# Optimization experiments

Measured on AMD Instinct MI355X. Metric: run time of the kernel, lower is better.

Reference implementation:

```python
import jax, jax.numpy as jnp
import numpy as np
import math

N_FEATURES = 64
GAMMA_ORDER = 0.5
ALPHA, BETA, ETA = 0.3, 0.4, 0.3
MAX_K = 50


def _make_coeffs():
    # gamma_values[0] = Gamma(g+1); gamma_values[m] (m>=1) = Gamma(m)*Gamma(g-m+2)
    g0 = math.gamma(GAMMA_ORDER + 1.0)
    coeffs = np.zeros(MAX_K + 1, dtype=np.float32)
    coeffs[0] = 1.0
    for k in range(1, MAX_K + 1):
        gv_k = math.gamma(k) * math.gamma(GAMMA_ORDER - k + 2.0)
        coeffs[k] = ((-1.0) ** k) * g0 / gv_k
    return jnp.asarray(coeffs)


def setup_inputs() -> dict:
    key = jax.random.key(0)
    k1, k2, k3, k4 = jax.random.split(key, 4)
    B, T, F = 4, 8192, N_FEATURES
    x = jax.random.normal(k1, (B, T, F), dtype=jnp.float32)
    weight_matrix = jax.random.normal(k2, (F, F), dtype=jnp.float32)
    bound = 1.0 / math.sqrt(F)
    proj_w = jax.random.uniform(k3, (F, F), dtype=jnp.float32, minval=-bound, maxval=bound)
    proj_b = jax.random.uniform(k4, (F,), dtype=jnp.float32, minval=-bound, maxval=bound)
    kappa = jnp.float32(0.1)
    coeffs = _make_coeffs()
    return {"x": x, "weight_matrix": weight_matrix, "proj_w": proj_w,
            "proj_b": proj_b, "kappa": kappa, "coeffs": coeffs}


def _fractional_derivative(x, coeffs):
    # causal conv: result[:, t, :] = sum_{k=0}^{min(t, max_k)} coeffs[k] * x[:, t-k, :]
    K = coeffs.shape[0]
    F = x.shape[-1]
    # depthwise 1D cross-correlation; kernel reversed so it implements x[t-k]
    kern = jnp.tile(coeffs[::-1][:, None, None], (1, 1, F))  # [K, 1, F]
    return jax.lax.conv_general_dilated(
        x, kern, window_strides=(1,), padding=[(K - 1, 0)],
        dimension_numbers=("NWC", "WIO", "NWC"), feature_group_count=F)


def reference(x, weight_matrix, proj_w, proj_b, kappa, coeffs):
    B, T, F = x.shape
    # 1) memory term: fractional derivative (causal conv)
    memory_term = _fractional_derivative(x, coeffs)

    # 2) coupling term: sum_j w[i,j] * tanh(x_i - x_j) * sigmoid(|x_i| + |x_j|)
    #    diagonal contributes tanh(0)=0, matching the i != j skip in the original.
    w = jax.nn.softmax(weight_matrix, axis=1)                 # [F, F]
    xi = x[..., :, None]                                      # [B, T, F, 1]
    xj = x[..., None, :]                                      # [B, T, 1, F]
    c = jnp.tanh(xi - xj) * jax.nn.sigmoid(jnp.abs(xi) + jnp.abs(xj))  # [B,T,F,F]
    coupling_term = jnp.einsum("btij,ij->bti", c, w)

    # 3) global term: proj(x[:, t]) * sum_{s=0}^{t} exp(-kappa * s)
    proj = x @ proj_w.T + proj_b                               # [B, T, F]
    kernel_cumsum = jnp.cumsum(jnp.exp(-kappa * jnp.arange(T, dtype=x.dtype)))
    global_term = proj * kernel_cumsum[None, :, None]

    output = ALPHA * memory_term + BETA * coupling_term + ETA * global_term
    return (output, memory_term)
```

## Files before the change

kernel.cpp:

```cpp
#include <hip/hip_runtime.h>
#include <hip/hip_fp16.h>
#include <math.h>

#define TT 8192
#define FF 64
#define TILE 64
#define HALO 50

typedef float f32x2 __attribute__((ext_vector_type(2)));
typedef float f32x4 __attribute__((ext_vector_type(4)));

__device__ __forceinline__ float rcpf(float x) { return __builtin_amdgcn_rcpf(x); }

__global__ void prep_kernel(const float* __restrict__ W, const float* __restrict__ PW,
                            float* __restrict__ wsmT, float* __restrict__ pwT) {
    const int lane = threadIdx.x;
    const int wv   = threadIdx.y;
    for (int it = 0; it < 16; ++it) {
        const int r = wv * 16 + it;
        float v = W[r * 64 + lane];
        float m = v;
        #pragma unroll
        for (int off = 32; off >= 1; off >>= 1)
            m = fmaxf(m, __shfl_xor(m, off, 64));
        float e = __expf(v - m);
        float s = e;
        #pragma unroll
        for (int off = 32; off >= 1; off >>= 1)
            s += __shfl_xor(s, off, 64);
        wsmT[lane * 64 + r] = e * rcpf(s);
        pwT[lane * 64 + r]  = PW[r * 64 + lane];
    }
}

__global__ __launch_bounds__(1024, 8)
void mcao_main(const float* __restrict__ x,
               const float* __restrict__ wsmT,
               const float* __restrict__ pwT,
               const float* __restrict__ pb,
               const float* __restrict__ kap,
               const float* __restrict__ coeffs,
               float* __restrict__ out,
               float* __restrict__ memout) {
    __shared__ __align__(16) char smem[66048];
    float* xs  = (float*)smem;
    f32x2* tux = (f32x2*)smem;
    float* P2  = (float*)smem;
    float* wS  = (float*)(smem + 33280);
    float* pwS = (float*)(smem + 49664);

    const int tid  = threadIdx.x;
    const int lane = tid & 63;
    const int wv   = tid >> 6;

    const int sw = ((int)blockIdx.x & 7) * 64 + ((int)blockIdx.x >> 3);
    const int b  = sw >> 7;
    const int t0 = (sw & 127) * TILE;
    const float* xb = x + (size_t)b * TT * FF;

    #pragma unroll
    for (int k = 0; k < 2; ++k) {
        const int i4 = tid + 1024 * k;
        if (i4 < 114 * 16) {
            const int s = i4 >> 4, f4 = i4 & 15, t = t0 - HALO + s;
            f32x4 v = {0.f, 0.f, 0.f, 0.f};
            if (t >= 0) v = *(const f32x4*)(xb + (size_t)t * 64 + f4 * 4);
            *(f32x4*)(&xs[s * 64 + f4 * 4]) = v;
        }
    }
    ((f32x4*)wS)[tid]  = ((const f32x4*)wsmT)[tid];
    ((f32x4*)pwS)[tid] = ((const f32x4*)pwT)[tid];
    __syncthreads();

    float macc[4] = {0.f, 0.f, 0.f, 0.f};
    #pragma unroll
    for (int s = 0; s < 54; ++s) {
        const float xv = xs[(4 * wv + s) * 64 + lane];
        #pragma unroll
        for (int r = 0; r < 4; ++r) {
            const int k = r + 50 - s;
            if (0 <= k && k <= 50) macc[r] = fmaf(coeffs[k], xv, macc[r]);
        }
    }
    #pragma unroll
    for (int r = 0; r < 4; ++r)
        memout[(size_t)(b * TT + t0 + 4 * wv + r) * 64 + lane] = macc[r];

    const int erow = tid >> 4, f0 = (tid & 15) * 4;
    const f32x4 xv4 = *(const f32x4*)(&xs[(HALO + erow) * 64 + f0]);
    float tq[4]; unsigned pk[4];
    #pragma unroll
    for (int q = 0; q < 4; ++q) {
        const float xi = xv4[q];
        tq[q] = fmaf(-2.f, rcpf(__expf(2.f * xi) + 1.f), 1.f);
        const float uu = __expf(-fabsf(xi));
        pk[q] = (unsigned)__half_as_ushort(__float2half_rn(xi)) << 16 |
                (unsigned)__half_as_ushort(__float2half_rn(uu));
    }
    __syncthreads();
    #pragma unroll
    for (int q = 0; q < 4; ++q) {
        f32x2 e; e.x = tq[q]; e.y = __uint_as_float(pk[q]);
        tux[(f0 + q) * 65 + erow] = e;
    }
    __syncthreads();

    const int r  = lane;
    const int ib = __builtin_amdgcn_readfirstlane(wv) * 4;

    f32x2 tiP[2], uiP[2];
    #pragma unroll
    for (int q = 0; q < 4; ++q) {
        const f32x2 e = tux[(ib + q) * 65 + r];
        const unsigned u = __float_as_uint(e.y);
        tiP[q >> 1][q & 1] = e.x;
        uiP[q >> 1][q & 1] = __half2float(__ushort_as_half((unsigned short)(u & 0xFFFF)));
    }

    f32x2 cac[2] = {{0.f, 0.f}, {0.f, 0.f}};
    f32x2 pac[2] = {{0.f, 0.f}, {0.f, 0.f}};
    const f32x2 one2 = {1.f, 1.f};
    #pragma unroll 8
    for (int j = 0; j < 64; ++j) {
        const f32x2 e = tux[j * 65 + r];
        const unsigned u = __float_as_uint(e.y);
        const float tj = e.x;
        const float uj = __half2float(__ushort_as_half((unsigned short)(u & 0xFFFF)));
        const float xj = __half2float(__ushort_as_half((unsigned short)(u >> 16)));
        const f32x4 w4 = *(const f32x4*)(wS  + j * 64 + ib);
        const f32x4 p4 = *(const f32x4*)(pwS + j * 64 + ib);
        const f32x2 tjj = {tj, tj}, ujj = {uj, uj}, xjj = {xj, xj};
        #pragma unroll
        for (int g = 0; g < 2; ++g) {
            const f32x2 d1  = __builtin_elementwise_fma(-tiP[g], tjj, one2);
            const f32x2 d2  = __builtin_elementwise_fma( uiP[g], ujj, one2);
            const f32x2 den = d1 * d2;
            f32x2 rr; rr.x = rcpf(den.x); rr.y = rcpf(den.y);
            const f32x2 s = (tiP[g] - tjj) * rr;
            f32x2 wg; wg.x = w4[2 * g]; wg.y = w4[2 * g + 1];
            f32x2 pg; pg.x = p4[2 * g]; pg.y = p4[2 * g + 1];
            cac[g] = __builtin_elementwise_fma(s,   wg, cac[g]);
            pac[g] = __builtin_elementwise_fma(xjj, pg, pac[g]);
        }
    }

    const float kappa  = kap[0];
    const float inv1mr = rcpf(1.f - __expf(-kappa));
    const float ksum   = (1.f - __expf(-kappa * (float)(t0 + r + 1))) * inv1mr;
    const f32x4 pbv    = *(const f32x4*)(pb + ib);
    __syncthreads();
    #pragma unroll
    for (int q = 0; q < 4; ++q) {
        const float cv = (q & 1) ? cac[q >> 1].y : cac[q >> 1].x;
        const float pv = (q & 1) ? pac[q >> 1].y : pac[q >> 1].x;
        P2[(ib + q) * 65 + r] = fmaf(0.4f, cv, 0.3f * (pv + pbv[q]) * ksum);
    }
    __syncthreads();

    #pragma unroll
    for (int rr2 = 0; rr2 < 4; ++rr2) {
        const int row = 4 * wv + rr2;
        out[(size_t)(b * TT + t0 + row) * 64 + lane] =
            fmaf(0.3f, macc[rr2], P2[lane * 65 + row]);
    }
}

extern "C" void kernel_launch(void* const* d_in, const int* in_sizes, int n_in,
                              void* d_out, int out_size, void* d_ws, size_t ws_size,
                              hipStream_t stream) {
    const float* x   = (const float*)d_in[0];
    const float* W   = (const float*)d_in[1];
    const float* PW  = (const float*)d_in[2];
    const float* pb  = (const float*)d_in[3];
    const float* kap = (const float*)d_in[4];
    const float* cf  = (const float*)d_in[5];

    float* out    = (float*)d_out;
    float* memout = out + (size_t)4 * TT * FF;

    float* wsmT = (float*)d_ws;
    float* pwT  = wsmT + 64 * 64;

    hipLaunchKernelGGL(prep_kernel, dim3(1), dim3(64, 4), 0, stream, W, PW, wsmT, pwT);
    hipLaunchKernelGGL(mcao_main, dim3(4 * (TT / TILE)), dim3(1024), 0, stream,
                       x, wsmT, pwT, pb, kap, cf, out, memout);
}
```

Baseline: 48.42 us.

## Compute projection with fp16 MFMA, halve tile size, keep coupling inputs in fp32

Moves the x @ proj_w^T projection out of the scalar inner loop onto 16x16x32 fp16 MFMA instructions, using a B-fragment layout pre-packed by the prep kernel. The tile shrinks from 64 to 32 timesteps with 512-thread blocks, so the grid doubles and LDS use drops, and the P2 buffer switches to an XOR-swizzled layout. tanh and exp(-|x|) are now stored as fp32 rather than packed halves, so the coupling inputs keep full precision. The cost is fp16 rounding of x and proj_w in the projection, plus more halo reloading per output row because the tile is smaller.

```diff
diff --git a/kernel.cpp b/kernel.cpp
--- a/kernel.cpp
+++ b/kernel.cpp
@@ -4,18 +4,21 @@
 
 #define TT 8192
 #define FF 64
-#define TILE 64
+#define TILE 32
 #define HALO 50
 
 typedef float f32x2 __attribute__((ext_vector_type(2)));
 typedef float f32x4 __attribute__((ext_vector_type(4)));
+typedef _Float16 f16x8 __attribute__((ext_vector_type(8)));
+typedef unsigned int u32x4 __attribute__((ext_vector_type(4)));
 
 __device__ __forceinline__ float rcpf(float x) { return __builtin_amdgcn_rcpf(x); }
 
 __global__ void prep_kernel(const float* __restrict__ W, const float* __restrict__ PW,
-                            float* __restrict__ wsmT, float* __restrict__ pwT) {
+                            float* __restrict__ wsmT, u32x4* __restrict__ pwB) {
     const int lane = threadIdx.x;
     const int wv   = threadIdx.y;
+    const int tid  = wv * 64 + lane;
     for (int it = 0; it < 16; ++it) {
         const int r = wv * 16 + it;
         float v = W[r * 64 + lane];
@@ -29,47 +32,55 @@
         for (int off = 32; off >= 1; off >>= 1)
             s += __shfl_xor(s, off, 64);
         wsmT[lane * 64 + r] = e * rcpf(s);
-        pwT[lane * 64 + r]  = PW[r * 64 + lane];
+    }
+    for (int s = tid; s < 512; s += 256) {
+        const int n2 = s >> 6;
+        const int ln = s & 63;
+        const int i  = (n2 >> 1) * 16 + (ln & 15);
+        const int k0 = (n2 & 1) * 32 + (ln >> 4) * 8;
+        u32x4 frag;
+        #pragma unroll
+        for (int w = 0; w < 4; ++w) {
+            const unsigned lo = __half_as_ushort(__float2half_rn(PW[i * 64 + k0 + 2 * w]));
+            const unsigned hi = __half_as_ushort(__float2half_rn(PW[i * 64 + k0 + 2 * w + 1]));
+            frag[w] = lo | (hi << 16);
+        }
+        pwB[s] = frag;
     }
 }
 
-__global__ __launch_bounds__(1024, 8)
+__global__ __launch_bounds__(512, 4)
 void mcao_main(const float* __restrict__ x,
                const float* __restrict__ wsmT,
-               const float* __restrict__ pwT,
+               const u32x4* __restrict__ pwB,
                const float* __restrict__ pb,
                const float* __restrict__ kap,
                const float* __restrict__ coeffs,
                float* __restrict__ out,
                float* __restrict__ memout) {
-    __shared__ __align__(16) char smem[66048];
+    __shared__ __align__(16) char smem[40960];
     float* xs  = (float*)smem;
     f32x2* tux = (f32x2*)smem;
-    float* P2  = (float*)smem;
-    float* wS  = (float*)(smem + 33280);
-    float* pwS = (float*)(smem + 49664);
+    float* P2  = (float*)(smem + 16384);
+    float* wS  = (float*)(smem + 24576);
 
     const int tid  = threadIdx.x;
     const int lane = tid & 63;
     const int wv   = tid >> 6;
 
-    const int sw = ((int)blockIdx.x & 7) * 64 + ((int)blockIdx.x >> 3);
-    const int b  = sw >> 7;
-    const int t0 = (sw & 127) * TILE;
+    const int sw = ((int)blockIdx.x & 7) * 128 + ((int)blockIdx.x >> 3);
+    const int b  = sw >> 8;
+    const int t0 = (sw & 255) * TILE;
     const float* xb = x + (size_t)b * TT * FF;
 
-    #pragma unroll
-    for (int k = 0; k < 2; ++k) {
-        const int i4 = tid + 1024 * k;
-        if (i4 < 114 * 16) {
-            const int s = i4 >> 4, f4 = i4 & 15, t = t0 - HALO + s;
-            f32x4 v = {0.f, 0.f, 0.f, 0.f};
-            if (t >= 0) v = *(const f32x4*)(xb + (size_t)t * 64 + f4 * 4);
-            *(f32x4*)(&xs[s * 64 + f4 * 4]) = v;
-        }
-    }
-    ((f32x4*)wS)[tid]  = ((const f32x4*)wsmT)[tid];
-    ((f32x4*)pwS)[tid] = ((const f32x4*)pwT)[tid];
+    for (int i4 = tid; i4 < 82 * 16; i4 += 512) {
+        const int s = i4 >> 4, f4 = i4 & 15, t = t0 - HALO + s;
+        f32x4 v = {0.f, 0.f, 0.f, 0.f};
+        if (t >= 0) v = *(const f32x4*)(xb + (size_t)t * 64 + f4 * 4);
+        *(f32x4*)(&xs[i4 * 4]) = v;
+    }
+    ((f32x4*)wS)[tid]       = ((const f32x4*)wsmT)[tid];
+    ((f32x4*)wS)[tid + 512] = ((const f32x4*)wsmT)[tid + 512];
     __syncthreads();
 
     float macc[4] = {0.f, 0.f, 0.f, 0.f};
@@ -88,72 +99,97 @@
 
     const int erow = tid >> 4, f0 = (tid & 15) * 4;
     const f32x4 xv4 = *(const f32x4*)(&xs[(HALO + erow) * 64 + f0]);
-    float tq[4]; unsigned pk[4];
+    f32x2 tu[4];
     #pragma unroll
     for (int q = 0; q < 4; ++q) {
         const float xi = xv4[q];
-        tq[q] = fmaf(-2.f, rcpf(__expf(2.f * xi) + 1.f), 1.f);
-        const float uu = __expf(-fabsf(xi));
-        pk[q] = (unsigned)__half_as_ushort(__float2half_rn(xi)) << 16 |
-                (unsigned)__half_as_ushort(__float2half_rn(uu));
-    }
-    __syncthreads();
+        tu[q].x = fmaf(-2.f, rcpf(__expf(2.f * xi) + 1.f), 1.f);
+        tu[q].y = __expf(-fabsf(xi));
+    }
+
+    const int mt = wv >> 2, nt = wv & 3;
+    const int arow = HALO + mt * 16 + (lane & 15);
+    const int kcol = (lane >> 4) * 8;
+    f32x4 cfr = {0.f, 0.f, 0.f, 0.f};
+    #pragma unroll
+    for (int kt = 0; kt < 2; ++kt) {
+        const f32x4 alo = *(const f32x4*)(&xs[arow * 64 + kt * 32 + kcol]);
+        const f32x4 ahi = *(const f32x4*)(&xs[arow * 64 + kt * 32 + kcol + 4]);
+        f16x8 afr;
+        #pragma unroll
+        for (int q = 0; q < 4; ++q) {
+            afr[q]     = (_Float16)alo[q];
+            afr[q + 4] = (_Float16)ahi[q];
+        }
+        const u32x4 bw = pwB[(nt * 2 + kt) * 64 + lane];
+        const f16x8 bfr = __builtin_bit_cast(f16x8, bw);
+        cfr = __builtin_amdgcn_mfma_f32_16x16x32_f16(afr, bfr, cfr, 0, 0, 0);
+    }
+    __syncthreads();
+
+    #pragma unroll
+    for (int q = 0; q < 4; ++q)
+        tux[(f0 + q) * 32 + erow] = tu[q];
+    {
+        const int ic = nt * 16 + (lane & 15);
+        const int rbase = mt * 16 + (lane >> 4) * 4;
+        #pragma unroll
+        for (int reg = 0; reg < 4; ++reg) {
+            const int rr = rbase + reg;
+            P2[ic * 32 + (rr ^ (ic & 31))] = cfr[reg];
+        }
+    }
+    __syncthreads();
+
+    const int r  = lane & 31;
+    const int h  = lane >> 5;
+    const int ib = wv * 8 + h * 4;
+    f32x2 tiP[2], uiP[2];
     #pragma unroll
     for (int q = 0; q < 4; ++q) {
-        f32x2 e; e.x = tq[q]; e.y = __uint_as_float(pk[q]);
-        tux[(f0 + q) * 65 + erow] = e;
-    }
-    __syncthreads();
-
-    const int r  = lane;
-    const int ib = __builtin_amdgcn_readfirstlane(wv) * 4;
-
-    f32x2 tiP[2], uiP[2];
-    #pragma unroll
-    for (int q = 0; q < 4; ++q) {
-        const f32x2 e = tux[(ib + q) * 65 + r];
-        const unsigned u = __float_as_uint(e.y);
+        const f32x2 e = tux[(ib + q) * 32 + r];
         tiP[q >> 1][q & 1] = e.x;
-        uiP[q >> 1][q & 1] = __half2float(__ushort_as_half((unsigned short)(u & 0xFFFF)));
-    }
-
-    f32x2 cac[2] = {{0.f, 0.f}, {0.f, 0.f}};
-    f32x2 pac[2] = {{0.f, 0.f}, {0.f, 0.f}};
+        uiP[q >> 1][q & 1] = e.y;
+    }
+
+    f32x2 cac0 = {0.f, 0.f}, cac1 = {0.f, 0.f};
     const f32x2 one2 = {1.f, 1.f};
     #pragma unroll 8
     for (int j = 0; j < 64; ++j) {
-        const f32x2 e = tux[j * 65 + r];
-        const unsigned u = __float_as_uint(e.y);
-        const float tj = e.x;
-        const float uj = __half2float(__ushort_as_half((unsigned short)(u & 0xFFFF)));
-        const float xj = __half2float(__ushort_as_half((unsigned short)(u >> 16)));
-        const f32x4 w4 = *(const f32x4*)(wS  + j * 64 + ib);
-        const f32x4 p4 = *(const f32x4*)(pwS + j * 64 + ib);
-        const f32x2 tjj = {tj, tj}, ujj = {uj, uj}, xjj = {xj, xj};
-        #pragma unroll
-        for (int g = 0; g < 2; ++g) {
-            const f32x2 d1  = __builtin_elementwise_fma(-tiP[g], tjj, one2);
-            const f32x2 d2  = __builtin_elementwise_fma( uiP[g], ujj, one2);
+        const f32x2 e  = tux[j * 32 + r];
+        const f32x4 w4 = *(const f32x4*)(&wS[j * 64 + ib]);
+        const f32x2 tjj = {e.x, e.x}, ujj = {e.y, e.y};
+        {
+            const f32x2 d1  = __builtin_elementwise_fma(-tiP[0], tjj, one2);
+            const f32x2 d2  = __builtin_elementwise_fma( uiP[0], ujj, one2);
             const f32x2 den = d1 * d2;
-            f32x2 rr; rr.x = rcpf(den.x); rr.y = rcpf(den.y);
-            const f32x2 s = (tiP[g] - tjj) * rr;
-            f32x2 wg; wg.x = w4[2 * g]; wg.y = w4[2 * g + 1];
-            f32x2 pg; pg.x = p4[2 * g]; pg.y = p4[2 * g + 1];
-            cac[g] = __builtin_elementwise_fma(s,   wg, cac[g]);
-            pac[g] = __builtin_elementwise_fma(xjj, pg, pac[g]);
-        }
-    }
-
-    const float kappa  = kap[0];
-    const float inv1mr = rcpf(1.f - __expf(-kappa));
-    const float ksum   = (1.f - __expf(-kappa * (float)(t0 + r + 1))) * inv1mr;
-    const f32x4 pbv    = *(const f32x4*)(pb + ib);
-    __syncthreads();
+            f32x2 rr0; rr0.x = rcpf(den.x); rr0.y = rcpf(den.y);
+            const f32x2 s0 = (tiP[0] - tjj) * rr0;
+            f32x2 w0; w0.x = w4[0]; w0.y = w4[1];
+            cac0 = __builtin_elementwise_fma(s0, w0, cac0);
+        }
+        {
+            const f32x2 d1  = __builtin_elementwise_fma(-tiP[1], tjj, one2);
+            const f32x2 d2  = __builtin_elementwise_fma( uiP[1], ujj, one2);
+            const f32x2 den = d1 * d2;
+            f32x2 rr1; rr1.x = rcpf(den.x); rr1.y = rcpf(den.y);
+            const f32x2 s1 = (tiP[1] - tjj) * rr1;
+            f32x2 w1; w1.x = w4[2]; w1.y = w4[3];
+            cac1 = __builtin_elementwise_fma(s1, w1, cac1);
+        }
+    }
+
+    const float kappa = kap[0];
+    const float ksum  = (1.f - __expf(-kappa * (float)(t0 + r + 1))) *
+                        rcpf(1.f - __expf(-kappa));
+    const f32x4 pbv = *(const f32x4*)(pb + ib);
     #pragma unroll
     for (int q = 0; q < 4; ++q) {
-        const float cv = (q & 1) ? cac[q >> 1].y : cac[q >> 1].x;
-        const float pv = (q & 1) ? pac[q >> 1].y : pac[q >> 1].x;
-        P2[(ib + q) * 65 + r] = fmaf(0.4f, cv, 0.3f * (pv + pbv[q]) * ksum);
+        const float cv = (q & 1) ? ((q >> 1) ? cac1.y : cac0.y)
+                                 : ((q >> 1) ? cac1.x : cac0.x);
+        const int ic  = ib + q;
+        const int idx = ic * 32 + (r ^ (ic & 31));
+        P2[idx] = fmaf(0.4f, cv, 0.3f * (P2[idx] + pbv[q]) * ksum);
     }
     __syncthreads();
 
@@ -161,7 +197,7 @@
     for (int rr2 = 0; rr2 < 4; ++rr2) {
         const int row = 4 * wv + rr2;
         out[(size_t)(b * TT + t0 + row) * 64 + lane] =
-            fmaf(0.3f, macc[rr2], P2[lane * 65 + row]);
+            fmaf(0.3f, macc[rr2], P2[lane * 32 + (row ^ (lane & 31))]);
     }
 }
 
@@ -179,9 +215,9 @@
     float* memout = out + (size_t)4 * TT * FF;
 
     float* wsmT = (float*)d_ws;
-    float* pwT  = wsmT + 64 * 64;
-
-    hipLaunchKernelGGL(prep_kernel, dim3(1), dim3(64, 4), 0, stream, W, PW, wsmT, pwT);
-    hipLaunchKernelGGL(mcao_main, dim3(4 * (TT / TILE)), dim3(1024), 0, stream,
-                       x, wsmT, pwT, pb, kap, cf, out, memout);
+    u32x4* pwB  = (u32x4*)((char*)d_ws + 16384);
+
+    hipLaunchKernelGGL(prep_kernel, dim3(1), dim3(64, 4), 0, stream, W, PW, wsmT, pwB);
+    hipLaunchKernelGGL(mcao_main, dim3(4 * (TT / TILE)), dim3(512), 0, stream,
+                       x, wsmT, pwB, pb, kap, cf, out, memout);
 }
```

Measured after the change: 45.36 us. 1.07x faster.
